# Optimization experiments

Hardware: AMD Instinct MI355X
Metric: run time of the kernel (lower is better)

Reference implementation:

```python
import jax, jax.numpy as jnp
import numpy as np

MARGIN = 0.3
POS_THRESH_M = 25.0
NEG_THRESH_M = 100.0
EARTH_R = 6371000.0
B, D = 1024, 256


def _pairwise_haversine(gps):
    # gps: [B,2] degrees -> [B,B] meters
    lat = jnp.deg2rad(gps[:, 0])
    dlat = jnp.deg2rad(gps[None, :, 0] - gps[:, None, 0])
    dlon = jnp.deg2rad(gps[None, :, 1] - gps[:, None, 1])
    a = jnp.sin(dlat / 2) ** 2 + jnp.cos(lat)[:, None] * jnp.cos(lat)[None, :] * jnp.sin(dlon / 2) ** 2
    return EARTH_R * 2.0 * jnp.arctan2(jnp.sqrt(a), jnp.sqrt(1.0 - a))


def _pairwise_euclidean(emb):
    # faithful to torch.norm(emb[None]-emb[:,None], dim=-1), with safe sqrt at 0
    diff = emb[None, :, :] - emb[:, None, :]          # [B,B,D]
    sq = jnp.sum(diff * diff, axis=-1)                # [B,B]
    return jnp.where(sq > 0, jnp.sqrt(jnp.where(sq > 0, sq, 1.0)), 0.0)


def setup_inputs() -> dict:
    key = jax.random.key(0)
    k1, k2 = jax.random.split(key)
    embeddings = jax.random.normal(k1, (B, D), dtype=jnp.float32)
    # small geographic box (~222 m x ~182 m) so both positive (<25 m) and
    # negative (>100 m) pairs exist for nearly every anchor
    base = jnp.array([35.0, 139.0], dtype=jnp.float32)
    gps_coords = base + jax.random.uniform(k2, (B, 2), dtype=jnp.float32) * 0.002
    return {"embeddings": embeddings, "gps_coords": gps_coords}


def reference(embeddings, gps_coords):
    n = embeddings.shape[0]
    gps_d = _pairwise_haversine(gps_coords)           # [B,B]
    emb_d = _pairwise_euclidean(embeddings)           # [B,B]
    eye = jnp.eye(n, dtype=bool)
    pos_mask = (gps_d < POS_THRESH_M) & ~eye
    neg_mask = gps_d > NEG_THRESH_M

    has_pos = jnp.any(pos_mask, axis=1)
    has_neg = jnp.any(neg_mask, axis=1)
    valid = has_pos & has_neg                         # anchors contributing a triplet

    # hardest positive per anchor (masked max)
    d_ap = jnp.max(jnp.where(pos_mask, emb_d, -1.0), axis=1)          # [B]

    # semi-hard negatives: d_ap < d < d_ap + margin among negatives
    semi_mask = neg_mask & (emb_d > d_ap[:, None]) & (emb_d < d_ap[:, None] + MARGIN)
    has_semi = jnp.any(semi_mask, axis=1)
    BIG = jnp.float32(1e9)
    semi_min = jnp.min(jnp.where(semi_mask, emb_d, BIG), axis=1)
    neg_min = jnp.min(jnp.where(neg_mask, emb_d, BIG), axis=1)        # fallback: hardest negative
    d_an = jnp.where(has_semi, semi_min, neg_min)

    triplet = jax.nn.relu(d_ap - d_an + MARGIN)
    triplet = jnp.where(valid, triplet, 0.0)
    n_triplets = jnp.sum(valid.astype(jnp.float32))
    loss = jnp.sum(triplet) / jnp.maximum(n_triplets, 1.0)
    return loss
```

## Files before the change

### kernel.cpp

```cpp
#include <hip/hip_runtime.h>

#define NB 1024
#define ND 256
#define APB 8
#define JCH 256
#define NTHR 256
#define MARGINF 0.3f
#define BIGV 1e9f
#define D2R 0.017453292519943295f
#define HD2R 0.008726646259971648f

#define A_POS 3.8495040e-12f
#define A_NEG 6.1592064e-11f

__device__ __forceinline__ float d4(float4 a, float4 b, float acc) {
    return fmaf(a.x,b.x, fmaf(a.y,b.y, fmaf(a.z,b.z, fmaf(a.w,b.w, acc))));
}

__device__ __forceinline__ float reduce4(const float v[4], int lane) {
    const bool b0 = lane & 1, b1 = lane & 2;
    float n1[2];
    #pragma unroll
    for (int i = 0; i < 2; ++i) {
        float sv = b0 ? v[i]   : v[2+i];
        float kp = b0 ? v[2+i] : v[i];
        n1[i] = kp + __shfl_xor(sv, 1);
    }
    float sv = b1 ? n1[0] : n1[1];
    float kp = b1 ? n1[1] : n1[0];
    float n2 = kp + __shfl_xor(sv, 2);
    return n2 + __shfl_xor(n2, 4);
}

__global__ __launch_bounds__(256) void prep_kernel(
    const float* __restrict__ emb, const float* __restrict__ gps,
    float4* __restrict__ prep)
{
    const int tid = threadIdx.x;
    const int row = blockIdx.x*16 + (tid >> 4);
    const int kk  = tid & 15;
    const float4* r4 = (const float4*)emb + (size_t)row*64;
    float s = 0.f;
    #pragma unroll
    for (int c = 0; c < 4; ++c) { float4 v = r4[kk + 16*c]; s = d4(v, v, s); }
    #pragma unroll
    for (int off = 1; off < 16; off <<= 1) s += __shfl_xor(s, off);
    if (kk == 0) {
        float2 g = ((const float2*)gps)[row];
        prep[row] = make_float4(s, g.x, g.y, cosf(g.x * D2R));
    }
}

__global__ __launch_bounds__(NTHR, 2) void gram_kernel(
    const float* __restrict__ emb, const float4* __restrict__ prep,
    float* __restrict__ sEnc, float* __restrict__ pP)
{
    __shared__ float sPm[4][APB];

    const int tid  = threadIdx.x;
    const int lane = tid & 63;
    const int w    = tid >> 6;
    const int jj   = lane >> 3;
    const int kk   = lane & 7;
    const int ah   = (w >> 1) * 4;
    const int a    = ah + 2*(lane & 1) + ((lane >> 1) & 1);
    const int ig   = blockIdx.x >> 2;
    const int c    = blockIdx.x & 3;
    const int i0   = ig * APB;
    const int jbase = c * JCH;
    const float4* __restrict__ emb4 = (const float4*)emb;

    float4 cA[4][8];
    #pragma unroll
    for (int ai = 0; ai < 4; ++ai)
        #pragma unroll
        for (int q = 0; q < 8; ++q)
            cA[ai][q] = emb4[(size_t)(i0+ah+ai)*64 + kk + 8*q];

    const float4 pa = prep[i0 + a];
    const float SA = pa.x, latA = pa.y, lonA = pa.z, cosA = pa.w;

    float pmax = -1.f;

    int jr = jbase + (w & 1)*8 + jj;
    float4 v[8];
    #pragma unroll
    for (int q = 0; q < 8; ++q) v[q] = emb4[(size_t)jr*64 + kk + 8*q];
    float4 pv = prep[jr];

    #pragma unroll 2
    for (int t = 0; t < 16; ++t) {
        float4 wv[8]; float4 pw;
        int jr2 = jbase + (t+1)*16 + (w & 1)*8 + jj;
        if (t < 15) {
            #pragma unroll
            for (int q = 0; q < 8; ++q) wv[q] = emb4[(size_t)jr2*64 + kk + 8*q];
            pw = prep[jr2];
        }
        float ac[4];
        #pragma unroll
        for (int ai = 0; ai < 4; ++ai) {
            float s = 0.f;
            #pragma unroll
            for (int q = 0; q < 8; ++q) s = d4(v[q], cA[ai][q], s);
            ac[ai] = s;
        }
        const float dot = reduce4(ac, lane);

        float d2v = SA + pv.x - 2.f*dot;
        d2v = d2v > 0.f ? d2v : 0.f;

        const float sla = sinf((pv.y - latA) * HD2R);
        const float slo = sinf((pv.z - lonA) * HD2R);
        const float hav = fmaf(sla, sla, (cosA * pv.w) * (slo*slo));
        const bool pos = (hav < A_POS) && (jr != i0 + a);
        const bool neg = (hav > A_NEG);

        pmax = fmaxf(pmax, pos ? d2v : -1.f);
        if (!(lane & 4))
            sEnc[(size_t)(i0+a)*NB + jr] = neg ? d2v : BIGV;

        jr = jr2; pv = pw;
        #pragma unroll
        for (int q = 0; q < 8; ++q) v[q] = wv[q];
    }

    #pragma unroll
    for (int off = 4; off < 64; off <<= 1) pmax = fmaxf(pmax, __shfl_xor(pmax, off));
    if (lane < 4) sPm[w][a] = pmax;
    __syncthreads();
    if (tid < 8) {
        const int w0 = (tid < 4) ? 0 : 2;
        pP[(i0 + tid)*4 + c] = fmaxf(sPm[w0][tid], sPm[w0+1][tid]);
    }
}

__global__ __launch_bounds__(256) void rows_kernel(
    const float* __restrict__ sEnc, const float* __restrict__ pP,
    float* __restrict__ tri, float* __restrict__ val)
{
    const int tid = threadIdx.x, lane = tid & 63, w = tid >> 6;
    const int i = blockIdx.x*4 + w;

    const float dap2 = fmaxf(fmaxf(pP[i*4+0], pP[i*4+1]), fmaxf(pP[i*4+2], pP[i*4+3]));
    const bool has_pos = dap2 > -0.5f;
    float lo2 = -1.f, hi2 = -1.f;
    if (has_pos) { const float hb = sqrtf(dap2) + MARGINF; lo2 = dap2; hi2 = hb*hb; }

    float nmin = BIGV, smin = BIGV;
    const float4* __restrict__ row = (const float4*)sEnc + (size_t)i*256;
    #pragma unroll
    for (int p = 0; p < 4; ++p) {
        const float4 x = row[p*64 + lane];
        #pragma unroll
        for (int q = 0; q < 4; ++q) {
            const float xc = (q==0) ? x.x : (q==1) ? x.y : (q==2) ? x.z : x.w;
            nmin = fminf(nmin, xc);
            smin = fminf(smin, (xc > lo2 && xc < hi2) ? xc : BIGV);
        }
    }
    #pragma unroll
    for (int off = 1; off < 64; off <<= 1) {
        nmin = fminf(nmin, __shfl_xor(nmin, off));
        smin = fminf(smin, __shfl_xor(smin, off));
    }
    if (lane == 0) {
        const bool has_neg  = nmin < 0.5f*BIGV;
        const bool has_semi = smin < 0.5f*BIGV;
        const float dan2 = has_semi ? smin : nmin;
        const float dap  = has_pos ? sqrtf(dap2) : 0.f;
        float t = dap - sqrtf(dan2) + MARGINF;
        t = t > 0.f ? t : 0.f;
        const bool valid = has_pos && has_neg;
        tri[i] = valid ? t : 0.f;
        val[i] = valid ? 1.f : 0.f;
    }
}

__global__ __launch_bounds__(256) void finalize_kernel(
    const float* __restrict__ tri, const float* __restrict__ val, float* __restrict__ out)
{
    const int tid = threadIdx.x;
    float st = 0.f, sv = 0.f;
    #pragma unroll
    for (int g = 0; g < 4; ++g) { st += tri[tid + (g<<8)]; sv += val[tid + (g<<8)]; }
    #pragma unroll
    for (int off = 1; off < 64; off <<= 1) { st += __shfl_xor(st, off); sv += __shfl_xor(sv, off); }
    __shared__ float rt[4], rv[4];
    if ((tid & 63) == 0) { rt[tid>>6] = st; rv[tid>>6] = sv; }
    __syncthreads();
    if (tid == 0) {
        float t = rt[0]+rt[1]+rt[2]+rt[3];
        float v = rv[0]+rv[1]+rv[2]+rv[3];
        out[0] = t / fmaxf(v, 1.f);
    }
}

extern "C" void kernel_launch(void* const* d_in, const int* in_sizes, int n_in,
                              void* d_out, int out_size, void* d_ws, size_t ws_size,
                              hipStream_t stream) {
    const float* emb = (const float*)d_in[0];
    const float* gps = (const float*)d_in[1];
    float* ws = (float*)d_ws;

    float*  sEnc = ws;
    float4* prep = (float4*)(ws + 1048576);
    float*  pP   = ws + 1048576 + 4096;
    float*  tri  = pP + 4096;
    float*  val  = tri + 1024;

    prep_kernel<<<64, 256, 0, stream>>>(emb, gps, prep);
    gram_kernel<<<512, NTHR, 0, stream>>>(emb, prep, sEnc, pP);
    rows_kernel<<<256, 256, 0, stream>>>(sEnc, pP, tri, val);
    finalize_kernel<<<1, 256, 0, stream>>>(tri, val, (float*)d_out);
}
```

Baseline: 32.62 us.

## Compute Gram matrix with bf16 MFMA on hi/lo split embeddings

Measured after the change: 28.58 us. -12.4%, faster.

```diff
diff --git a/kernel.cpp b/kernel.cpp
--- a/kernel.cpp
+++ b/kernel.cpp
@@ -1,10 +1,12 @@
 #include <hip/hip_runtime.h>
+#include <hip/hip_bf16.h>
+
+typedef __attribute__((ext_vector_type(8))) short bf16x8;
+typedef __attribute__((ext_vector_type(4))) float f32x4;
 
 #define NB 1024
 #define ND 256
-#define APB 8
-#define JCH 256
-#define NTHR 256
+#define KC 512
 #define MARGINF 0.3f
 #define BIGV 1e9f
 #define D2R 0.017453292519943295f
@@ -17,24 +19,9 @@
     return fmaf(a.x,b.x, fmaf(a.y,b.y, fmaf(a.z,b.z, fmaf(a.w,b.w, acc))));
 }
 
-__device__ __forceinline__ float reduce4(const float v[4], int lane) {
-    const bool b0 = lane & 1, b1 = lane & 2;
-    float n1[2];
-    #pragma unroll
-    for (int i = 0; i < 2; ++i) {
-        float sv = b0 ? v[i]   : v[2+i];
-        float kp = b0 ? v[2+i] : v[i];
-        n1[i] = kp + __shfl_xor(sv, 1);
-    }
-    float sv = b1 ? n1[0] : n1[1];
-    float kp = b1 ? n1[1] : n1[0];
-    float n2 = kp + __shfl_xor(sv, 2);
-    return n2 + __shfl_xor(n2, 4);
-}
-
 __global__ __launch_bounds__(256) void prep_kernel(
     const float* __restrict__ emb, const float* __restrict__ gps,
-    float4* __restrict__ prep)
+    float4* __restrict__ prep, unsigned short* __restrict__ C)
 {
     const int tid = threadIdx.x;
     const int row = blockIdx.x*16 + (tid >> 4);
@@ -42,7 +29,22 @@
     const float4* r4 = (const float4*)emb + (size_t)row*64;
     float s = 0.f;
     #pragma unroll
-    for (int c = 0; c < 4; ++c) { float4 v = r4[kk + 16*c]; s = d4(v, v, s); }
+    for (int c = 0; c < 4; ++c) {
+        float4 v = r4[kk + 16*c];
+        s = d4(v, v, s);
+        float fv[4] = {v.x, v.y, v.z, v.w};
+        unsigned short hh[4], ll[4];
+        #pragma unroll
+        for (int q = 0; q < 4; ++q) {
+            __hip_bfloat16 hb = __float2bfloat16(fv[q]);
+            float hf = __bfloat162float(hb);
+            __hip_bfloat16 lb = __float2bfloat16(fv[q] - hf);
+            hh[q] = *(unsigned short*)&hb;
+            ll[q] = *(unsigned short*)&lb;
+        }
+        *(ushort4*)(C + (size_t)row*KC +       4*(kk+16*c)) = make_ushort4(hh[0],hh[1],hh[2],hh[3]);
+        *(ushort4*)(C + (size_t)row*KC + 256 + 4*(kk+16*c)) = make_ushort4(ll[0],ll[1],ll[2],ll[3]);
+    }
     #pragma unroll
     for (int off = 1; off < 16; off <<= 1) s += __shfl_xor(s, off);
     if (kk == 0) {
@@ -51,87 +53,66 @@
     }
 }
 
-__global__ __launch_bounds__(NTHR, 2) void gram_kernel(
-    const float* __restrict__ emb, const float4* __restrict__ prep,
+__global__ __launch_bounds__(256) void gram_mfma(
+    const unsigned short* __restrict__ C, const float4* __restrict__ prep,
     float* __restrict__ sEnc, float* __restrict__ pP)
 {
-    __shared__ float sPm[4][APB];
-
-    const int tid  = threadIdx.x;
-    const int lane = tid & 63;
-    const int w    = tid >> 6;
-    const int jj   = lane >> 3;
-    const int kk   = lane & 7;
-    const int ah   = (w >> 1) * 4;
-    const int a    = ah + 2*(lane & 1) + ((lane >> 1) & 1);
-    const int ig   = blockIdx.x >> 2;
-    const int c    = blockIdx.x & 3;
-    const int i0   = ig * APB;
-    const int jbase = c * JCH;
-    const float4* __restrict__ emb4 = (const float4*)emb;
-
-    float4 cA[4][8];
-    #pragma unroll
-    for (int ai = 0; ai < 4; ++ai)
-        #pragma unroll
-        for (int q = 0; q < 8; ++q)
-            cA[ai][q] = emb4[(size_t)(i0+ah+ai)*64 + kk + 8*q];
-
-    const float4 pa = prep[i0 + a];
-    const float SA = pa.x, latA = pa.y, lonA = pa.z, cosA = pa.w;
-
-    float pmax = -1.f;
-
-    int jr = jbase + (w & 1)*8 + jj;
-    float4 v[8];
-    #pragma unroll
-    for (int q = 0; q < 8; ++q) v[q] = emb4[(size_t)jr*64 + kk + 8*q];
-    float4 pv = prep[jr];
-
-    #pragma unroll 2
-    for (int t = 0; t < 16; ++t) {
-        float4 wv[8]; float4 pw;
-        int jr2 = jbase + (t+1)*16 + (w & 1)*8 + jj;
-        if (t < 15) {
+    __shared__ float sRed[64][33];
+
+    const int tid = threadIdx.x, lane = tid & 63, w = tid >> 6;
+    const int wr = w >> 1, wc = w & 1;
+    const int ib = blockIdx.x & 15, jb = blockIdx.x >> 4;
+    const int i0 = ib*64, j0 = jb*64;
+    const int lr = lane & 15, lk = lane >> 4;
+    const short* Cs = (const short*)C;
+
+    f32x4 acc[2][2] = {};
+    #pragma unroll 4
+    for (int ks = 0; ks < 16; ++ks) {
+        bf16x8 a0 = *(const bf16x8*)(Cs + (size_t)(i0 + wr*32      + lr)*KC + ks*32 + lk*8);
+        bf16x8 a1 = *(const bf16x8*)(Cs + (size_t)(i0 + wr*32 + 16 + lr)*KC + ks*32 + lk*8);
+        bf16x8 b0 = *(const bf16x8*)(Cs + (size_t)(j0 + wc*32      + lr)*KC + ks*32 + lk*8);
+        bf16x8 b1 = *(const bf16x8*)(Cs + (size_t)(j0 + wc*32 + 16 + lr)*KC + ks*32 + lk*8);
+        acc[0][0] = __builtin_amdgcn_mfma_f32_16x16x32_bf16(a0, b0, acc[0][0], 0, 0, 0);
+        acc[0][1] = __builtin_amdgcn_mfma_f32_16x16x32_bf16(a0, b1, acc[0][1], 0, 0, 0);
+        acc[1][0] = __builtin_amdgcn_mfma_f32_16x16x32_bf16(a1, b0, acc[1][0], 0, 0, 0);
+        acc[1][1] = __builtin_amdgcn_mfma_f32_16x16x32_bf16(a1, b1, acc[1][1], 0, 0, 0);
+    }
+
+    float4 pj[2];
+    pj[0] = prep[j0 + wc*32 + lr];
+    pj[1] = prep[j0 + wc*32 + 16 + lr];
+
+    #pragma unroll
+    for (int fi = 0; fi < 2; ++fi) {
+        #pragma unroll
+        for (int r = 0; r < 4; ++r) {
+            const int rl = wr*32 + fi*16 + lk*4 + r;
+            const int gi = i0 + rl;
+            const float4 pi = prep[gi];
+            float pmax = -1.f;
             #pragma unroll
-            for (int q = 0; q < 8; ++q) wv[q] = emb4[(size_t)jr2*64 + kk + 8*q];
-            pw = prep[jr2];
+            for (int fj = 0; fj < 2; ++fj) {
+                const int gj = j0 + wc*32 + fj*16 + lr;
+                float d2v = pi.x + pj[fj].x - 2.f*acc[fi][fj][r];
+                d2v = d2v > 0.f ? d2v : 0.f;
+                const float sla = sinf((pj[fj].y - pi.y) * HD2R);
+                const float slo = sinf((pj[fj].z - pi.z) * HD2R);
+                const float hav = fmaf(sla, sla, (pi.w * pj[fj].w) * (slo*slo));
+                const bool pos = (hav < A_POS) && (gi != gj);
+                const bool neg = (hav > A_NEG);
+                pmax = fmaxf(pmax, pos ? d2v : -1.f);
+                sEnc[(size_t)gi*NB + gj] = neg ? d2v : BIGV;
+            }
+            sRed[rl][lr + 16*wc] = pmax;
         }
-        float ac[4];
-        #pragma unroll
-        for (int ai = 0; ai < 4; ++ai) {
-            float s = 0.f;
-            #pragma unroll
-            for (int q = 0; q < 8; ++q) s = d4(v[q], cA[ai][q], s);
-            ac[ai] = s;
-        }
-        const float dot = reduce4(ac, lane);
-
-        float d2v = SA + pv.x - 2.f*dot;
-        d2v = d2v > 0.f ? d2v : 0.f;
-
-        const float sla = sinf((pv.y - latA) * HD2R);
-        const float slo = sinf((pv.z - lonA) * HD2R);
-        const float hav = fmaf(sla, sla, (cosA * pv.w) * (slo*slo));
-        const bool pos = (hav < A_POS) && (jr != i0 + a);
-        const bool neg = (hav > A_NEG);
-
-        pmax = fmaxf(pmax, pos ? d2v : -1.f);
-        if (!(lane & 4))
-            sEnc[(size_t)(i0+a)*NB + jr] = neg ? d2v : BIGV;
-
-        jr = jr2; pv = pw;
-        #pragma unroll
-        for (int q = 0; q < 8; ++q) v[q] = wv[q];
-    }
-
-    #pragma unroll
-    for (int off = 4; off < 64; off <<= 1) pmax = fmaxf(pmax, __shfl_xor(pmax, off));
-    if (lane < 4) sPm[w][a] = pmax;
+    }
     __syncthreads();
-    if (tid < 8) {
-        const int w0 = (tid < 4) ? 0 : 2;
-        pP[(i0 + tid)*4 + c] = fmaxf(sPm[w0][tid], sPm[w0+1][tid]);
+    if (tid < 64) {
+        float m = sRed[tid][0];
+        #pragma unroll
+        for (int c = 1; c < 32; ++c) m = fmaxf(m, sRed[tid][c]);
+        pP[(i0 + tid)*16 + jb] = m;
     }
 }
 
@@ -142,7 +123,10 @@
     const int tid = threadIdx.x, lane = tid & 63, w = tid >> 6;
     const int i = blockIdx.x*4 + w;
 
-    const float dap2 = fmaxf(fmaxf(pP[i*4+0], pP[i*4+1]), fmaxf(pP[i*4+2], pP[i*4+3]));
+    float p = pP[i*16 + (lane & 15)];
+    #pragma unroll
+    for (int off = 1; off < 16; off <<= 1) p = fmaxf(p, __shfl_xor(p, off));
+    const float dap2 = p;
     const bool has_pos = dap2 > -0.5f;
     float lo2 = -1.f, hi2 = -1.f;
     if (has_pos) { const float hb = sqrtf(dap2) + MARGINF; lo2 = dap2; hi2 = hb*hb; }
@@ -150,8 +134,8 @@
     float nmin = BIGV, smin = BIGV;
     const float4* __restrict__ row = (const float4*)sEnc + (size_t)i*256;
     #pragma unroll
-    for (int p = 0; p < 4; ++p) {
-        const float4 x = row[p*64 + lane];
+    for (int pss = 0; pss < 4; ++pss) {
+        const float4 x = row[pss*64 + lane];
         #pragma unroll
         for (int q = 0; q < 4; ++q) {
             const float xc = (q==0) ? x.x : (q==1) ? x.y : (q==2) ? x.z : x.w;
@@ -203,14 +187,15 @@
     const float* gps = (const float*)d_in[1];
     float* ws = (float*)d_ws;
 
-    float*  sEnc = ws;
-    float4* prep = (float4*)(ws + 1048576);
-    float*  pP   = ws + 1048576 + 4096;
-    float*  tri  = pP + 4096;
-    float*  val  = tri + 1024;
-
-    prep_kernel<<<64, 256, 0, stream>>>(emb, gps, prep);
-    gram_kernel<<<512, NTHR, 0, stream>>>(emb, prep, sEnc, pP);
+    float*          sEnc = ws;
+    unsigned short* Cbf  = (unsigned short*)(ws + 1048576);
+    float4*         prep = (float4*)(ws + 1048576 + 262144);
+    float*          pP   = ws + 1048576 + 262144 + 4096;
+    float*          tri  = pP + 16384;
+    float*          val  = tri + 1024;
+
+    prep_kernel<<<64, 256, 0, stream>>>(emb, gps, prep, Cbf);
+    gram_mfma<<<256, 256, 0, stream>>>(Cbf, prep, sEnc, pP);
     rows_kernel<<<256, 256, 0, stream>>>(sEnc, pP, tri, val);
     finalize_kernel<<<1, 256, 0, stream>>>(tri, val, (float*)d_out);
 }
```
